# Kernel optimization log

Measured on AMD Instinct MI355X. Metric: run time of the kernel, lower is better.

Reference implementation:

```python
import jax, jax.numpy as jnp
import numpy as np

# Dims: B=batch, S=seq, H=hidden, I=intermediate, E=experts, K=top-k
B, S, H, I, E, K = 1, 1024, 1024, 1024, 8, 2


def setup_inputs() -> dict:
    key = jax.random.key(0)
    k0, k1, k2, k3 = jax.random.split(key, 4)
    return {
        "hidden_states": jax.random.normal(k0, (B, S, H), dtype=jnp.float32),
        "router_weight": jax.random.normal(k1, (E, H), dtype=jnp.float32) * 0.02,
        "gate_up_proj": jax.random.normal(k2, (E, H, 2 * I), dtype=jnp.float32) * 0.02,
        "gate_up_proj_bias": jnp.zeros((E, 2 * I), dtype=jnp.float32),
        "down_proj": jax.random.normal(k3, (E, I, H), dtype=jnp.float32) * 0.02,
        "down_proj_bias": jnp.zeros((E, H), dtype=jnp.float32),
    }


def reference(hidden_states, router_weight, gate_up_proj, gate_up_proj_bias,
              down_proj, down_proj_bias):
    b, s, h = hidden_states.shape
    flat = hidden_states.reshape(b * s, h)            # [N, H]
    n = flat.shape[0]

    # Router: softmax over experts, then top-k selection
    logits = flat @ router_weight.T                   # [N, E]
    scores = jax.nn.softmax(logits, axis=-1)          # [N, E]
    _, indices = jax.lax.top_k(scores, K)             # [N, K]

    # Dense all-experts GEMM (matches original: every token through every expert)
    gate_up = jnp.einsum('nh,eho->neo', flat, gate_up_proj) + gate_up_proj_bias  # [N, E, 2I]
    gate = jnp.minimum(gate_up[..., ::2], 7.0)        # interleaved gate, clamp max
    up = jnp.clip(gate_up[..., 1::2], -7.0, 7.0)      # interleaved up, clamp both
    activated = (up + 1.0) * gate * jax.nn.sigmoid(gate * 1.702)  # [N, E, I]

    expert_out = jnp.einsum('nei,eih->neh', activated, down_proj) + down_proj_bias  # [N, E, H]

    # Masked combine: zero weights except at top-k experts
    top_w = jnp.take_along_axis(scores, indices, axis=-1)                     # [N, K]
    weights = jnp.zeros_like(scores).at[jnp.arange(n)[:, None], indices].set(top_w)  # [N, E]
    out = (expert_out * weights[..., None]).sum(axis=1)                       # [N, H]
    return out.reshape(b, s, h), scores
```

## Files before the change

### kernel.cpp

```cpp
#include <hip/hip_runtime.h>
#include <hip/hip_bf16.h>

typedef __attribute__((ext_vector_type(8))) short short8;
typedef __attribute__((ext_vector_type(4))) float f32x4;

#define NTOK 1024
#define HDIM 1024
#define IDIM 1024
#define NEXP 8
#define NCOL 2048

#define WS_COUNTS   0
#define WS_Q        960
#define WS_LTOK     1024
#define WS_LW       (WS_LTOK + NEXP*NTOK*4)
#define WS_XBF      131072
#define WS_ACT      (WS_XBF + NTOK*HDIM*2)
#define WS_W1B      (WS_ACT + 2*NTOK*IDIM*2)
#define WS_W2B      (WS_W1B + (size_t)NEXP*NCOL*HDIM*2)

static __device__ __forceinline__ unsigned short f2bf(float x) {
    __hip_bfloat16 h = __float2bfloat16(x);
    return __builtin_bit_cast(unsigned short, h);
}

#define GLDS16(g, l) __builtin_amdgcn_global_load_lds( \
    (const __attribute__((address_space(1))) void*)(g), \
    (__attribute__((address_space(3))) void*)(l), 16, 0, 0)

static __device__ __forceinline__ float4 xpose4(float4 v, int i) {
    float x = (i & 1) ? v.x : v.y;
    float y = (i & 1) ? v.z : v.w;
    x = __shfl_xor(x, 1); y = __shfl_xor(y, 1);
    if (i & 1) { v.x = x; v.z = y; } else { v.y = x; v.w = y; }
    float x2 = (i & 2) ? v.x : v.z;
    float y2 = (i & 2) ? v.y : v.w;
    x2 = __shfl_xor(x2, 2); y2 = __shfl_xor(y2, 2);
    if (i & 2) { v.x = x2; v.y = y2; } else { v.z = x2; v.w = y2; }
    return v;
}

__global__ __launch_bounds__(256) void prep_kernel(
    const float* __restrict__ flat, const float* __restrict__ rw,
    const float* __restrict__ gup,
    float* __restrict__ scores, int* __restrict__ counts,
    int* __restrict__ ltok, float* __restrict__ lw,
    unsigned short* __restrict__ xbf, unsigned short* __restrict__ w1b)
{
    __shared__ unsigned short tile[64][70];
    const int b = blockIdx.x;
    const int t = threadIdx.x;

    if (b >= 256) {
        const int tid = b - 256;
        const int e = tid >> 9, rem = tid & 511, kb = rem >> 5, cb = rem & 31;
        const int i4 = t & 3, g = t >> 2;
        const int rq = g >> 4, cq = (g & 15) * 4;
        const float* s0 = gup + ((size_t)e * 1024 + kb * 64 + rq * 16 + i4) * NCOL
                         + cb * 64 + cq;
        float4 vr[4];
#pragma unroll
        for (int it = 0; it < 4; ++it)
            vr[it] = *(const float4*)(s0 + (size_t)(it * 4) * NCOL);
        const int c = cq + i4;
#pragma unroll
        for (int it = 0; it < 4; ++it) {
            float4 v = xpose4(vr[it], i4);
            ushort4 o;
            o.x = f2bf(v.x); o.y = f2bf(v.y); o.z = f2bf(v.z); o.w = f2bf(v.w);
            *(ushort4*)&tile[c][rq * 16 + it * 4] = o;
        }
        __syncthreads();
        unsigned short* d0 = w1b + (((size_t)e * 16 + kb) * NCOL + cb * 64) * 64;
#pragma unroll
        for (int p = 0; p < 2; ++p) {
            int cc = p * 32 + (t >> 3), q = t & 7;
            short8 vv = *(const short8*)&tile[cc][q * 8];
            *(short8*)&d0[(size_t)cc * 64 + q * 8] = vv;
        }
        return;
    }

    const int n = b * 4 + (t >> 6);
    const int l = t & 63;
    float acc[NEXP];
#pragma unroll
    for (int e = 0; e < NEXP; ++e) acc[e] = 0.f;
    const float* xrow = flat + (size_t)n * HDIM;
#pragma unroll
    for (int j = 0; j < 4; ++j) {
        int h = j * 256 + l * 4;
        float4 v = *(const float4*)&xrow[h];
        ushort4 xb;
        xb.x = f2bf(v.x); xb.y = f2bf(v.y); xb.z = f2bf(v.z); xb.w = f2bf(v.w);
        *(ushort4*)&xbf[(size_t)n * HDIM + h] = xb;
#pragma unroll
        for (int e = 0; e < NEXP; ++e) {
            float4 wv = *(const float4*)&rw[e * HDIM + h];
            acc[e] += v.x * wv.x + v.y * wv.y + v.z * wv.z + v.w * wv.w;
        }
    }
#pragma unroll
    for (int e = 0; e < NEXP; ++e) {
#pragma unroll
        for (int off = 32; off > 0; off >>= 1)
            acc[e] += __shfl_down(acc[e], off);
    }
    if (l == 0) {
        float m = acc[0];
#pragma unroll
        for (int e = 1; e < NEXP; ++e) m = fmaxf(m, acc[e]);
        float s = 0.f, p[NEXP];
#pragma unroll
        for (int e = 0; e < NEXP; ++e) { p[e] = __expf(acc[e] - m); s += p[e]; }
        float inv = 1.f / s;
#pragma unroll
        for (int e = 0; e < NEXP; ++e) { p[e] *= inv; scores[n * NEXP + e] = p[e]; }
        int i0 = 0;
#pragma unroll
        for (int e = 1; e < NEXP; ++e) if (p[e] > p[i0]) i0 = e;
        int i1 = (i0 == 0) ? 1 : 0;
#pragma unroll
        for (int e = 0; e < NEXP; ++e) if (e != i0 && p[e] > p[i1]) i1 = e;
        int pos0 = atomicAdd(&counts[i0 * 32], 1);
        ltok[i0 * NTOK + pos0] = n; lw[i0 * NTOK + pos0] = p[i0];
        int pos1 = atomicAdd(&counts[i1 * 32], 1);
        ltok[i1 * NTOK + pos1] = n; lw[i1 * NTOK + pos1] = p[i1];
    }
}

__global__ __launch_bounds__(512) void gemm1_kernel(
    const unsigned short* __restrict__ xbf, const unsigned short* __restrict__ w1b,
    const float* __restrict__ gbias,
    const int* __restrict__ counts,
    const int* __restrict__ ltok, unsigned short* __restrict__ act,
    const float* __restrict__ dp, unsigned short* __restrict__ w2b,
    int* __restrict__ tq)
{
    const int lin = blockIdx.x + (blockIdx.y << 4) + (blockIdx.z << 7);
    const int nlin = ((lin & 7) << 7) + (lin >> 3);
    const int bx = nlin & 15, by = (nlin >> 4) & 7, e = nlin >> 7;

    int cnt = 0, off = 0;
#pragma unroll
    for (int j2 = 0; j2 < NEXP; ++j2) {
        int c = counts[j2 * 32];
        if (j2 < e) off += c;
        if (j2 == e) cnt = c;
    }
    const int t = threadIdx.x;

    __shared__ unsigned short As[2][128][64];
    __shared__ unsigned short Bs[2][128][64];
    __shared__ int toks[128];
    __shared__ int tbase;

    if (by * 128 >= cnt) {
        unsigned short (*ttile)[64][70] = (unsigned short (*)[64][70])(&As[0][0][0]);
        const int half = t >> 8, tt = t & 255;
        const int i4 = tt & 3, g = tt >> 2;
        const int rq = g >> 4, cq4 = (g & 15) * 4;
        for (;;) {
            if (t == 0) tbase = atomicAdd(tq, 2);
            __syncthreads();
            int base = tbase;
            if (base >= 2048) break;
            int myt = base + half;
            int te = myt >> 8, rem = myt & 255, kb = rem >> 4, cb = rem & 15;
            const float* s0 = dp + ((size_t)te * 1024 + kb * 64 + rq * 16 + i4) * HDIM
                             + cb * 64 + cq4;
            float4 vr[4];
#pragma unroll
            for (int it = 0; it < 4; ++it)
                vr[it] = *(const float4*)(s0 + (size_t)(it * 4) * HDIM);
            const int c = cq4 + i4;
#pragma unroll
            for (int it = 0; it < 4; ++it) {
                float4 v = xpose4(vr[it], i4);
                ushort4 o;
                o.x = f2bf(v.x); o.y = f2bf(v.y); o.z = f2bf(v.z); o.w = f2bf(v.w);
                *(ushort4*)&ttile[half][c][rq * 16 + it * 4] = o;
            }
            __syncthreads();
            unsigned short* d0 = w2b + (((size_t)te * 16 + kb) * HDIM + cb * 64) * 64;
#pragma unroll
            for (int p = 0; p < 2; ++p) {
                int cc = p * 32 + (tt >> 3), q = tt & 7;
                short8 vv = *(const short8*)&ttile[half][cc][q * 8];
                *(short8*)&d0[(size_t)cc * 64 + q * 8] = vv;
            }
        }
        return;
    }

    const int l = t & 63, w = t >> 6;
    const int wm = w >> 2, wn = w & 3;
    if (t < 128) toks[t] = ltok[e * NTOK + min(by * 128 + t, cnt - 1)];
    __syncthreads();

    const int li = l & 7, lr = l >> 3;
    const int kswz = (li ^ lr) * 8;
    const unsigned short* asrc[2];
    const unsigned short* bsrc[2];
#pragma unroll
    for (int j = 0; j < 2; ++j) {
        int rr = (w * 2 + j) * 8 + lr;
        asrc[j] = xbf + (size_t)toks[rr] * HDIM + kswz;
        bsrc[j] = w1b + (size_t)e * 16 * NCOL * 64 + (size_t)(bx * 128 + rr) * 64 + kswz;
    }

    f32x4 acc[4][2];
#pragma unroll
    for (int m = 0; m < 4; ++m)
#pragma unroll
        for (int n = 0; n < 2; ++n) acc[m][n] = 0.f;

#pragma unroll
    for (int j = 0; j < 2; ++j) {
        GLDS16(asrc[j], &As[0][(w * 2 + j) * 8][0]);
        GLDS16(bsrc[j], &Bs[0][(w * 2 + j) * 8][0]);
    }

    const int lg = l >> 4, lo = l & 15;
    const int cq0 = ((0 + lg) ^ (lo & 7)) * 8;
    const int cq1 = ((4 + lg) ^ (lo & 7)) * 8;

    for (int ks = 0; ks < HDIM / 64; ++ks) {
        const int p = ks & 1;
        __builtin_amdgcn_s_barrier();
        if (ks + 1 < HDIM / 64) {
            const int kadvA = (ks + 1) * 64;
            const size_t kadvB = (size_t)(ks + 1) * NCOL * 64;
#pragma unroll
            for (int j = 0; j < 2; ++j) {
                GLDS16(asrc[j] + kadvA, &As[p ^ 1][(w * 2 + j) * 8][0]);
                GLDS16(bsrc[j] + kadvB, &Bs[p ^ 1][(w * 2 + j) * 8][0]);
            }
            asm volatile("s_waitcnt vmcnt(4)" ::: "memory");
        } else {
            asm volatile("s_waitcnt vmcnt(0)" ::: "memory");
        }
        __builtin_amdgcn_sched_barrier(0);
        __builtin_amdgcn_s_barrier();
        __builtin_amdgcn_s_setprio(1);
#pragma unroll
        for (int q = 0; q < 2; ++q) {
            const int cq = q ? cq1 : cq0;
            short8 a0 = *(const short8*)&As[p][wm * 64 +  0 + lo][cq];
            short8 a1 = *(const short8*)&As[p][wm * 64 + 16 + lo][cq];
            short8 a2 = *(const short8*)&As[p][wm * 64 + 32 + lo][cq];
            short8 a3 = *(const short8*)&As[p][wm * 64 + 48 + lo][cq];
            short8 b0 = *(const short8*)&Bs[p][wn * 32 +  0 + lo][cq];
            short8 b1 = *(const short8*)&Bs[p][wn * 32 + 16 + lo][cq];
#pragma unroll
            for (int m = 0; m < 4; ++m) {
                short8 am = (m == 0) ? a0 : (m == 1) ? a1 : (m == 2) ? a2 : a3;
                acc[m][0] = __builtin_amdgcn_mfma_f32_16x16x32_bf16(am, b0, acc[m][0], 0, 0, 0);
                acc[m][1] = __builtin_amdgcn_mfma_f32_16x16x32_bf16(am, b1, acc[m][1], 0, 0, 0);
            }
        }
        __builtin_amdgcn_s_setprio(0);
    }

    const int rj = lg * 4;
#pragma unroll
    for (int m = 0; m < 4; ++m) {
#pragma unroll
        for (int n = 0; n < 2; ++n) {
            int col = bx * 128 + wn * 32 + n * 16 + lo;
            float bias = gbias[e * NCOL + col];
#pragma unroll
            for (int j = 0; j < 4; ++j) {
                int slot = by * 128 + wm * 64 + m * 16 + rj + j;
                float val = acc[m][n][j] + bias;
                float other = __shfl_xor(val, 1);
                float g = (l & 1) ? other : val;
                float u = (l & 1) ? val : other;
                g = fminf(g, 7.f);
                u = fminf(fmaxf(u, -7.f), 7.f);
                float av = (u + 1.f) * g * (1.f / (1.f + __expf(-1.702f * g)));
                if (!(l & 1) && slot < cnt)
                    act[(size_t)(off + slot) * IDIM + (col >> 1)] = f2bf(av);
            }
        }
    }
}

__global__ __launch_bounds__(512) void gemm2_kernel(
    const unsigned short* __restrict__ act, const unsigned short* __restrict__ w2b,
    const float* __restrict__ dbias,
    const int* __restrict__ counts,
    const int* __restrict__ ltok,
    const float* __restrict__ lw, float* __restrict__ outbuf)
{
    const int lin = blockIdx.x + (blockIdx.y << 4) + (blockIdx.z << 7);
    const int nlin = ((lin & 7) << 7) + (lin >> 3);
    const int bx = nlin & 15, by = (nlin >> 4) & 7, e = nlin >> 7;

    int cnt = 0, off = 0;
#pragma unroll
    for (int j2 = 0; j2 < NEXP; ++j2) {
        int c = counts[j2 * 32];
        if (j2 < e) off += c;
        if (j2 == e) cnt = c;
    }
    if (by * 128 >= cnt) return;
    const int t = threadIdx.x;
    const int l = t & 63, w = t >> 6;
    const int wm = w >> 1, wn = w & 1;

    __shared__ unsigned short As[2][128][64];
    __shared__ unsigned short Bs[2][64][64];
    __shared__ int toks[128];
    __shared__ float wts[128];
    if (t < 128) {
        int cl = min(by * 128 + t, cnt - 1);
        toks[t] = ltok[e * NTOK + cl];
        wts[t]  = lw[e * NTOK + cl];
    }
    __syncthreads();

    const int li = l & 7, lr = l >> 3;
    const int kswz = (li ^ lr) * 8;
    const unsigned short* asrc[2];
#pragma unroll
    for (int j = 0; j < 2; ++j) {
        int rr = (w * 2 + j) * 8 + lr;
        asrc[j] = act + (size_t)(off + min(by * 128 + rr, cnt - 1)) * IDIM + kswz;
    }
    const unsigned short* bsrc = w2b + (size_t)e * 16 * HDIM * 64
                               + (size_t)(bx * 64 + w * 8 + lr) * 64 + kswz;

    f32x4 acc[2][2];
#pragma unroll
    for (int m = 0; m < 2; ++m)
#pragma unroll
        for (int n = 0; n < 2; ++n) acc[m][n] = 0.f;

#pragma unroll
    for (int j = 0; j < 2; ++j)
        GLDS16(asrc[j], &As[0][(w * 2 + j) * 8][0]);
    GLDS16(bsrc, &Bs[0][w * 8][0]);

    const int lg = l >> 4, lo = l & 15;
    const int cq0 = ((0 + lg) ^ (lo & 7)) * 8;
    const int cq1 = ((4 + lg) ^ (lo & 7)) * 8;

    for (int ks = 0; ks < IDIM / 64; ++ks) {
        const int p = ks & 1;
        __builtin_amdgcn_s_barrier();
        if (ks + 1 < IDIM / 64) {
            const int kadvA = (ks + 1) * 64;
            const size_t kadvB = (size_t)(ks + 1) * HDIM * 64;
#pragma unroll
            for (int j = 0; j < 2; ++j)
                GLDS16(asrc[j] + kadvA, &As[p ^ 1][(w * 2 + j) * 8][0]);
            GLDS16(bsrc + kadvB, &Bs[p ^ 1][w * 8][0]);
            asm volatile("s_waitcnt vmcnt(3)" ::: "memory");
        } else {
            asm volatile("s_waitcnt vmcnt(0)" ::: "memory");
        }
        __builtin_amdgcn_sched_barrier(0);
        __builtin_amdgcn_s_barrier();
        __builtin_amdgcn_s_setprio(1);
#pragma unroll
        for (int q = 0; q < 2; ++q) {
            const int cq = q ? cq1 : cq0;
            short8 a0 = *(const short8*)&As[p][wm * 32 +  0 + lo][cq];
            short8 a1 = *(const short8*)&As[p][wm * 32 + 16 + lo][cq];
            short8 b0 = *(const short8*)&Bs[p][wn * 32 +  0 + lo][cq];
            short8 b1 = *(const short8*)&Bs[p][wn * 32 + 16 + lo][cq];
            acc[0][0] = __builtin_amdgcn_mfma_f32_16x16x32_bf16(a0, b0, acc[0][0], 0, 0, 0);
            acc[1][0] = __builtin_amdgcn_mfma_f32_16x16x32_bf16(a1, b0, acc[1][0], 0, 0, 0);
            acc[0][1] = __builtin_amdgcn_mfma_f32_16x16x32_bf16(a0, b1, acc[0][1], 0, 0, 0);
            acc[1][1] = __builtin_amdgcn_mfma_f32_16x16x32_bf16(a1, b1, acc[1][1], 0, 0, 0);
        }
        __builtin_amdgcn_s_setprio(0);
    }

    const int rj = lg * 4;
#pragma unroll
    for (int m = 0; m < 2; ++m) {
#pragma unroll
        for (int n = 0; n < 2; ++n) {
            int col = bx * 64 + wn * 32 + n * 16 + lo;
            float bias = dbias[e * HDIM + col];
#pragma unroll
            for (int j = 0; j < 4; ++j) {
                int sl = wm * 32 + m * 16 + rj + j;
                int slot = by * 128 + sl;
                if (slot < cnt) {
                    float val = (acc[m][n][j] + bias) * wts[sl];
                    atomicAdd(&outbuf[(size_t)toks[sl] * HDIM + col], val);
                }
            }
        }
    }
}

extern "C" void kernel_launch(void* const* d_in, const int* in_sizes, int n_in,
                              void* d_out, int out_size, void* d_ws, size_t ws_size,
                              hipStream_t stream) {
    const float* flat  = (const float*)d_in[0];
    const float* rw    = (const float*)d_in[1];
    const float* gup   = (const float*)d_in[2];
    const float* gbias = (const float*)d_in[3];
    const float* dp    = (const float*)d_in[4];
    const float* dbias = (const float*)d_in[5];
    float* out    = (float*)d_out;
    float* scores = out + (size_t)NTOK * HDIM;

    char* ws = (char*)d_ws;
    int*   counts  = (int*)(ws + WS_COUNTS);
    int*   tq      = (int*)(ws + WS_Q);
    int*   ltok    = (int*)(ws + WS_LTOK);
    float* lw      = (float*)(ws + WS_LW);
    unsigned short* xbf = (unsigned short*)(ws + WS_XBF);
    unsigned short* act = (unsigned short*)(ws + WS_ACT);
    unsigned short* w1b = (unsigned short*)(ws + WS_W1B);
    unsigned short* w2b = (unsigned short*)(ws + WS_W2B);

    hipMemsetAsync(ws, 0, 1024, stream);
    hipMemsetAsync(out, 0, (size_t)NTOK * HDIM * sizeof(float), stream);
    prep_kernel<<<4352, 256, 0, stream>>>(flat, rw, gup, scores, counts,
                                          ltok, lw, xbf, w1b);
    gemm1_kernel<<<dim3(16, 8, NEXP), 512, 0, stream>>>(xbf, w1b, gbias, counts,
                                                        ltok, act, dp, w2b, tq);
    gemm2_kernel<<<dim3(16, 8, NEXP), 512, 0, stream>>>(act, w2b, dbias, counts,
                                                        ltok, lw, out);
}
```

Baseline: 79.65 us.

## Split-K the first expert GEMM with atomic accumulation and a separate activation kernel

The first grouped GEMM's K dimension is split into two halves, doubling the grid so more blocks work on the routed tokens. Partial sums are added with fp32 atomics into a new zeroed workspace buffer. A new kernel then applies bias, clamping and the gated activation and writes the bf16 activations. The aim is better CU occupancy for the small per-expert M. In exchange it adds a large memset, atomic traffic, an extra launch and a full fp32 round trip. The idle blocks that run the weight-conversion branch are also duplicated across both K halves.

```diff
diff --git a/kernel.cpp b/kernel.cpp
--- a/kernel.cpp
+++ b/kernel.cpp
@@ -18,10 +18,17 @@
 #define WS_ACT      (WS_XBF + NTOK*HDIM*2)
 #define WS_W1B      (WS_ACT + 2*NTOK*IDIM*2)
 #define WS_W2B      (WS_W1B + (size_t)NEXP*NCOL*HDIM*2)
+#define WS_GACC     (WS_W2B + (size_t)NEXP*HDIM*IDIM*2)
 
 static __device__ __forceinline__ unsigned short f2bf(float x) {
     __hip_bfloat16 h = __float2bfloat16(x);
     return __builtin_bit_cast(unsigned short, h);
+}
+
+static __device__ __forceinline__ float actfn(float g, float u) {
+    g = fminf(g, 7.f);
+    u = fminf(fmaxf(u, -7.f), 7.f);
+    return (u + 1.f) * g * (1.f / (1.f + __expf(-1.702f * g)));
 }
 
 #define GLDS16(g, l) __builtin_amdgcn_global_load_lds( \
@@ -131,15 +138,15 @@
 
 __global__ __launch_bounds__(512) void gemm1_kernel(
     const unsigned short* __restrict__ xbf, const unsigned short* __restrict__ w1b,
-    const float* __restrict__ gbias,
     const int* __restrict__ counts,
-    const int* __restrict__ ltok, unsigned short* __restrict__ act,
+    const int* __restrict__ ltok, float* __restrict__ gacc,
     const float* __restrict__ dp, unsigned short* __restrict__ w2b,
     int* __restrict__ tq)
 {
-    const int lin = blockIdx.x + (blockIdx.y << 4) + (blockIdx.z << 7);
-    const int nlin = ((lin & 7) << 7) + (lin >> 3);
-    const int bx = nlin & 15, by = (nlin >> 4) & 7, e = nlin >> 7;
+    const int lin = blockIdx.x + (blockIdx.y << 4) + (blockIdx.z << 8);
+    const int nlin = ((lin & 7) << 8) + (lin >> 3);
+    const int bx = nlin & 15, yy = (nlin >> 4) & 15, e = nlin >> 8;
+    const int by = yy & 7, kh = yy >> 3;
 
     int cnt = 0, off = 0;
 #pragma unroll
@@ -205,8 +212,9 @@
 #pragma unroll
     for (int j = 0; j < 2; ++j) {
         int rr = (w * 2 + j) * 8 + lr;
-        asrc[j] = xbf + (size_t)toks[rr] * HDIM + kswz;
-        bsrc[j] = w1b + (size_t)e * 16 * NCOL * 64 + (size_t)(bx * 128 + rr) * 64 + kswz;
+        asrc[j] = xbf + (size_t)toks[rr] * HDIM + kh * 512 + kswz;
+        bsrc[j] = w1b + ((size_t)e * 16 + kh * 8) * NCOL * 64
+                + (size_t)(bx * 128 + rr) * 64 + kswz;
     }
 
     f32x4 acc[4][2];
@@ -225,10 +233,10 @@
     const int cq0 = ((0 + lg) ^ (lo & 7)) * 8;
     const int cq1 = ((4 + lg) ^ (lo & 7)) * 8;
 
-    for (int ks = 0; ks < HDIM / 64; ++ks) {
+    for (int ks = 0; ks < 8; ++ks) {
         const int p = ks & 1;
         __builtin_amdgcn_s_barrier();
-        if (ks + 1 < HDIM / 64) {
+        if (ks + 1 < 8) {
             const int kadvA = (ks + 1) * 64;
             const size_t kadvB = (size_t)(ks + 1) * NCOL * 64;
 #pragma unroll
@@ -268,22 +276,41 @@
 #pragma unroll
         for (int n = 0; n < 2; ++n) {
             int col = bx * 128 + wn * 32 + n * 16 + lo;
-            float bias = gbias[e * NCOL + col];
 #pragma unroll
             for (int j = 0; j < 4; ++j) {
                 int slot = by * 128 + wm * 64 + m * 16 + rj + j;
-                float val = acc[m][n][j] + bias;
-                float other = __shfl_xor(val, 1);
-                float g = (l & 1) ? other : val;
-                float u = (l & 1) ? val : other;
-                g = fminf(g, 7.f);
-                u = fminf(fmaxf(u, -7.f), 7.f);
-                float av = (u + 1.f) * g * (1.f / (1.f + __expf(-1.702f * g)));
-                if (!(l & 1) && slot < cnt)
-                    act[(size_t)(off + slot) * IDIM + (col >> 1)] = f2bf(av);
-            }
-        }
-    }
+                if (slot < cnt)
+                    atomicAdd(&gacc[(size_t)(off + slot) * NCOL + col], acc[m][n][j]);
+            }
+        }
+    }
+}
+
+__global__ __launch_bounds__(256) void act_kernel(
+    const float* __restrict__ gacc, const float* __restrict__ gbias,
+    const int* __restrict__ counts, unsigned short* __restrict__ act)
+{
+    const int slot = blockIdx.x;
+    int e = 0, acc0 = 0;
+#pragma unroll
+    for (int j = 0; j < NEXP; ++j) {
+        int c = counts[j * 32];
+        if (slot >= acc0 + c) { acc0 += c; e = j + 1; }
+    }
+    const int t = threadIdx.x;
+    const int i0 = t * 4;
+    const float* g0 = gacc + (size_t)slot * NCOL + i0 * 2;
+    float4 v0 = *(const float4*)(g0);
+    float4 v1 = *(const float4*)(g0 + 4);
+    const float* gb = gbias + (size_t)e * NCOL + i0 * 2;
+    float4 b0 = *(const float4*)(gb);
+    float4 b1 = *(const float4*)(gb + 4);
+    ushort4 o;
+    o.x = f2bf(actfn(v0.x + b0.x, v0.y + b0.y));
+    o.y = f2bf(actfn(v0.z + b0.z, v0.w + b0.w));
+    o.z = f2bf(actfn(v1.x + b1.x, v1.y + b1.y));
+    o.w = f2bf(actfn(v1.z + b1.z, v1.w + b1.w));
+    *(ushort4*)&act[(size_t)slot * IDIM + i0] = o;
 }
 
 __global__ __launch_bounds__(512) void gemm2_kernel(
@@ -419,13 +446,16 @@
     unsigned short* act = (unsigned short*)(ws + WS_ACT);
     unsigned short* w1b = (unsigned short*)(ws + WS_W1B);
     unsigned short* w2b = (unsigned short*)(ws + WS_W2B);
+    float* gacc    = (float*)(ws + WS_GACC);
 
     hipMemsetAsync(ws, 0, 1024, stream);
+    hipMemsetAsync(gacc, 0, (size_t)2048 * NCOL * sizeof(float), stream);
     hipMemsetAsync(out, 0, (size_t)NTOK * HDIM * sizeof(float), stream);
     prep_kernel<<<4352, 256, 0, stream>>>(flat, rw, gup, scores, counts,
                                           ltok, lw, xbf, w1b);
-    gemm1_kernel<<<dim3(16, 8, NEXP), 512, 0, stream>>>(xbf, w1b, gbias, counts,
-                                                        ltok, act, dp, w2b, tq);
+    gemm1_kernel<<<dim3(16, 16, NEXP), 512, 0, stream>>>(xbf, w1b, counts,
+                                                         ltok, gacc, dp, w2b, tq);
+    act_kernel<<<2048, 256, 0, stream>>>(gacc, gbias, counts, act);
     gemm2_kernel<<<dim3(16, 8, NEXP), 512, 0, stream>>>(act, w2b, dbias, counts,
                                                         ltok, lw, out);
 }
```

Result: slower. 113.7 us (+42.7%).
